# Optimization experiments

Hardware: AMD Instinct MI355X
Metric: run time of the kernel (lower is better)

Reference implementation:

```python
import jax, jax.numpy as jnp
import numpy as np

# Module configuration (matches init_kwargs)
B = 128           # batch
C = 21            # in_channels
L = 2048          # in_features
W = 32            # window_size
S = 8             # strides
O = 16            # out_channels
EPS = 1e-6
M = int((L - W) / S - EPS)      # number of regularly-strided windows (251)
NW = M + 1                       # total windows incl. clamped last one (252)
NK = O * NW                      # 4032
# window start positions: j*S for j<M, last window clamped to L-W
STARTS = np.concatenate([np.arange(M) * S, np.array([L - W])]).astype(np.int32)


def setup_inputs() -> dict:
    key = jax.random.key(0)
    kx, kw = jax.random.split(key)
    x = jax.random.normal(kx, (B, C, L), dtype=jnp.float32)
    # original init: 2*(rand-0.5)/sqrt(W*C), uniform in [-1,1]/sqrt(W*C)
    weight = (2.0 * (jax.random.uniform(kw, (NK, W * C), dtype=jnp.float32) - 0.5)
              / np.sqrt(W * C).astype(np.float32))
    return {"x": x, "weight": weight}


def reference(x, weight):
    # im2col gather implied by the sparse fbank: patches[b,c,j,w] = x[b,c,starts[j]+w]
    idx = jnp.asarray(STARTS)[:, None] + jnp.arange(W)[None, :]   # (NW, W)
    patches = x[:, :, idx]                                        # (B, C, NW, W)
    # weight rows are n = j*O + o, columns laid out k*W + w (channel-major)
    w4 = weight.reshape(NW, O, C, W)                              # (NW, O, C, W)
    # h[b, j*O+o] = sum_{c,w} patches[b,c,j,w] * w4[j,o,c,w]
    h = jnp.einsum('bcjw,jocw->bjo', patches, w4)                 # (B, NW, O)
    return h.reshape(B, NK)
```

## Files before the change

kernel.cpp:

```cpp
#include <hip/hip_runtime.h>
#include <hip/hip_bf16.h>

#define Bb   128
#define Cc   21
#define Ll   2048
#define Ss   8
#define Oo   16
#define NWw  252
#define NKk  4032
#define Kk   672
#define KP   680

typedef __attribute__((ext_vector_type(8))) short  short8;
typedef __attribute__((ext_vector_type(4))) float  f32x4;

static __device__ __forceinline__ unsigned short f2bf(float f) {
    union { __hip_bfloat16 h; unsigned short u; } cv;
    cv.h = __float2bfloat16(f);
    return cv.u;
}

__global__ __launch_bounds__(256)
void cvt_x(const float* __restrict__ x, unsigned short* __restrict__ xb) {
    const int total4 = Bb * Cc * Ll / 4;
    for (int t = blockIdx.x * 256 + threadIdx.x; t < total4;
         t += gridDim.x * 256) {
        float4 v = ((const float4*)x)[t];
        ushort4 p = make_ushort4(f2bf(v.x), f2bf(v.y), f2bf(v.z), f2bf(v.w));
        ((ushort4*)xb)[t] = p;
    }
}

__global__ __launch_bounds__(512)
void fb_mm(const unsigned short* __restrict__ xb, const float* __restrict__ w,
           float* __restrict__ out) {
    __shared__ unsigned short ws[Oo * KP];

    const int bid = blockIdx.x;
    const int j   = (bid & 7) * 32 + (bid >> 3);
    if (j >= NWw) return;
    const int s    = (j < NWw - 1) ? j * Ss : (Ll - 32);
    const int tid  = threadIdx.x;
    const int lane = tid & 63;
    const int wv   = tid >> 6;
    const int col  = lane & 15;
    const int quad = lane >> 4;

    {
        const float4* wj4 = (const float4*)(w + (size_t)j * Oo * Kk);
        for (int t = tid; t < Oo * (Kk / 4); t += 512) {
            float4 v = wj4[t];
            int o = t / (Kk / 4);
            int r = t - o * (Kk / 4);
            ushort4 p = make_ushort4(f2bf(v.x), f2bf(v.y), f2bf(v.z), f2bf(v.w));
            *(ushort4*)&ws[o * KP + r * 4] = p;
        }
    }

    const unsigned short* xrow =
        xb + ((size_t)(wv * 16 + col) * Cc) * Ll + s + quad * 8;
    short8 afr[Cc];
#pragma unroll
    for (int c = 0; c < Cc; ++c)
        afr[c] = *(const short8*)(xrow + (size_t)c * Ll);

    __syncthreads();

    const unsigned short* wrow = &ws[col * KP + quad * 8];
    f32x4 acc = {0.f, 0.f, 0.f, 0.f};
#pragma unroll
    for (int c = 0; c < Cc; ++c)
        acc = __builtin_amdgcn_mfma_f32_16x16x32_bf16(
            afr[c], *(const short8*)(wrow + c * 32), acc, 0, 0, 0);

    const int rbase = wv * 16 + quad * 4;
    float* op = out + (size_t)rbase * NKk + j * 16 + col;
#pragma unroll
    for (int r = 0; r < 4; ++r)
        op[(size_t)r * NKk] = acc[r];
}

extern "C" void kernel_launch(void* const* d_in, const int* in_sizes, int n_in,
                              void* d_out, int out_size, void* d_ws, size_t ws_size,
                              hipStream_t stream) {
    const float* x = (const float*)d_in[0];
    const float* w = (const float*)d_in[1];
    float* out = (float*)d_out;
    unsigned short* xb = (unsigned short*)d_ws;
    cvt_x<<<dim3(1344), dim3(256), 0, stream>>>(x, xb);
    fb_mm<<<dim3(256), dim3(512), 0, stream>>>(xb, w, out);
}
```

Measured before the change: 84.44 us.

## Pre-convert weights to bf16, DMA them into LDS, split batch across blocks

The weight fp32→bf16 conversion moves out of the matmul kernel into a combined conversion pre-pass that writes bf16 weights to workspace. The matmul kernel then fills LDS directly with global_load_lds 16-byte transfers, and the batch is split into two halves so twice as many 256-thread blocks run. The aim is to shorten the serial per-block weight staging and raise parallelism in the main kernel. The cost is an extra write and re-read of the bf16 weight copy, and each weight slice is now loaded by two blocks.

```diff
diff --git a/kernel.cpp b/kernel.cpp
--- a/kernel.cpp
+++ b/kernel.cpp
@@ -21,24 +21,35 @@
 }
 
 __global__ __launch_bounds__(256)
-void cvt_x(const float* __restrict__ x, unsigned short* __restrict__ xb) {
-    const int total4 = Bb * Cc * Ll / 4;
-    for (int t = blockIdx.x * 256 + threadIdx.x; t < total4;
-         t += gridDim.x * 256) {
+void cvt_all(const float* __restrict__ x, const float* __restrict__ w,
+             unsigned short* __restrict__ xb, unsigned short* __restrict__ wb) {
+    const int nx4 = Bb * Cc * Ll / 4;
+    const int nw4 = NKk * Kk / 4;
+    const int t0 = blockIdx.x * 256 + threadIdx.x;
+    const int st = gridDim.x * 256;
+    for (int t = t0; t < nx4; t += st) {
         float4 v = ((const float4*)x)[t];
-        ushort4 p = make_ushort4(f2bf(v.x), f2bf(v.y), f2bf(v.z), f2bf(v.w));
-        ((ushort4*)xb)[t] = p;
+        ((ushort4*)xb)[t] = make_ushort4(f2bf(v.x), f2bf(v.y), f2bf(v.z), f2bf(v.w));
+    }
+    for (int t = t0; t < nw4; t += st) {
+        float4 v = ((const float4*)w)[t];
+        ((ushort4*)wb)[t] = make_ushort4(f2bf(v.x), f2bf(v.y), f2bf(v.z), f2bf(v.w));
     }
 }
 
-__global__ __launch_bounds__(512)
-void fb_mm(const unsigned short* __restrict__ xb, const float* __restrict__ w,
+__global__ __launch_bounds__(256, 2)
+void fb_mm(const unsigned short* __restrict__ xb,
+           const unsigned short* __restrict__ wb,
            float* __restrict__ out) {
-    __shared__ unsigned short ws[Oo * KP];
+    __shared__ unsigned short ws[22 * 512];
 
     const int bid = blockIdx.x;
-    const int j   = (bid & 7) * 32 + (bid >> 3);
+    const int r   = bid & 7;
+    const int t2  = bid >> 3;
+    const int j   = r * 32 + (t2 >> 1);
+    const int bh  = t2 & 1;
     if (j >= NWw) return;
+
     const int s    = (j < NWw - 1) ? j * Ss : (Ll - 32);
     const int tid  = threadIdx.x;
     const int lane = tid & 63;
@@ -47,18 +58,21 @@
     const int quad = lane >> 4;
 
     {
-        const float4* wj4 = (const float4*)(w + (size_t)j * Oo * Kk);
-        for (int t = tid; t < Oo * (Kk / 4); t += 512) {
-            float4 v = wj4[t];
-            int o = t / (Kk / 4);
-            int r = t - o * (Kk / 4);
-            ushort4 p = make_ushort4(f2bf(v.x), f2bf(v.y), f2bf(v.z), f2bf(v.w));
-            *(ushort4*)&ws[o * KP + r * 4] = p;
+        const unsigned short* wj = wb + (size_t)j * (Oo * Kk);
+        for (int iss = wv; iss < 22; iss += 4) {
+            int g  = iss * 64 + lane;
+            int ro = g / 85;  if (ro > 15) ro = 15;
+            int co = g - ro * 85; if (co > 83) co = 83;
+            const unsigned short* src = wj + ro * Kk + co * 8;
+            __builtin_amdgcn_global_load_lds(
+                (const __attribute__((address_space(1))) void*)src,
+                (__attribute__((address_space(3))) void*)&ws[iss * 512],
+                16, 0, 0);
         }
     }
 
     const unsigned short* xrow =
-        xb + ((size_t)(wv * 16 + col) * Cc) * Ll + s + quad * 8;
+        xb + ((size_t)(bh * 64 + wv * 16 + col) * Cc) * Ll + s + quad * 8;
     short8 afr[Cc];
 #pragma unroll
     for (int c = 0; c < Cc; ++c)
@@ -73,11 +87,11 @@
         acc = __builtin_amdgcn_mfma_f32_16x16x32_bf16(
             afr[c], *(const short8*)(wrow + c * 32), acc, 0, 0, 0);
 
-    const int rbase = wv * 16 + quad * 4;
+    const int rbase = bh * 64 + wv * 16 + quad * 4;
     float* op = out + (size_t)rbase * NKk + j * 16 + col;
 #pragma unroll
-    for (int r = 0; r < 4; ++r)
-        op[(size_t)r * NKk] = acc[r];
+    for (int rr = 0; rr < 4; ++rr)
+        op[(size_t)rr * NKk] = acc[rr];
 }
 
 extern "C" void kernel_launch(void* const* d_in, const int* in_sizes, int n_in,
@@ -87,6 +101,7 @@
     const float* w = (const float*)d_in[1];
     float* out = (float*)d_out;
     unsigned short* xb = (unsigned short*)d_ws;
-    cvt_x<<<dim3(1344), dim3(256), 0, stream>>>(x, xb);
-    fb_mm<<<dim3(256), dim3(512), 0, stream>>>(xb, w, out);
+    unsigned short* wb = (unsigned short*)d_ws + (size_t)Bb * Cc * Ll;
+    cvt_all<<<dim3(2048), dim3(256), 0, stream>>>(x, w, xb, wb);
+    fb_mm<<<dim3(512), dim3(256), 0, stream>>>(xb, wb, out);
 }
```

Result: no change. 84.58 us (+0.2%).

## Transpose x into chunk-major bf16 layout so window loads are contiguous

Applied to the files above, without the earlier changes.

The conversion kernel now writes x as bf16 in an 8-element-chunk-major layout (chunk, row, 8), so each window's 32 samples across all batch/channel rows sit contiguously. The matmul kernel's A-fragment loads then read adjacent 16-byte pieces across lanes instead of strided rows, and they are issued before the weight staging so their latency overlaps it. The trade-off is that the transpose kernel's stores are now scattered with a large stride instead of streaming, and its grid is halved.

```diff
diff --git a/kernel.cpp b/kernel.cpp
--- a/kernel.cpp
+++ b/kernel.cpp
@@ -10,6 +10,8 @@
 #define NKk  4032
 #define Kk   672
 #define KP   680
+#define NR   (Bb * Cc)
+#define NCH  (Ll / 8)
 
 typedef __attribute__((ext_vector_type(8))) short  short8;
 typedef __attribute__((ext_vector_type(4))) float  f32x4;
@@ -21,18 +23,25 @@
 }
 
 __global__ __launch_bounds__(256)
-void cvt_x(const float* __restrict__ x, unsigned short* __restrict__ xb) {
-    const int total4 = Bb * Cc * Ll / 4;
-    for (int t = blockIdx.x * 256 + threadIdx.x; t < total4;
+void xpose(const float* __restrict__ x, unsigned short* __restrict__ xt) {
+    const int total = NR * NCH;
+    for (int t = blockIdx.x * 256 + threadIdx.x; t < total;
          t += gridDim.x * 256) {
-        float4 v = ((const float4*)x)[t];
-        ushort4 p = make_ushort4(f2bf(v.x), f2bf(v.y), f2bf(v.z), f2bf(v.w));
-        ((ushort4*)xb)[t] = p;
+        const int row = t >> 8;
+        const int k   = t & 255;
+        const float* src = x + (size_t)row * Ll + k * 8;
+        const float4 v0 = *(const float4*)src;
+        const float4 v1 = *(const float4*)(src + 4);
+        unsigned short* dst = xt + ((size_t)k * NR + row) * 8;
+        *(ushort4*)dst =
+            make_ushort4(f2bf(v0.x), f2bf(v0.y), f2bf(v0.z), f2bf(v0.w));
+        *(ushort4*)(dst + 4) =
+            make_ushort4(f2bf(v1.x), f2bf(v1.y), f2bf(v1.z), f2bf(v1.w));
     }
 }
 
 __global__ __launch_bounds__(512)
-void fb_mm(const unsigned short* __restrict__ xb, const float* __restrict__ w,
+void fb_mm(const unsigned short* __restrict__ xt, const float* __restrict__ w,
            float* __restrict__ out) {
     __shared__ unsigned short ws[Oo * KP];
 
@@ -40,11 +49,20 @@
     const int j   = (bid & 7) * 32 + (bid >> 3);
     if (j >= NWw) return;
     const int s    = (j < NWw - 1) ? j * Ss : (Ll - 32);
+    const int c0   = s >> 3;
     const int tid  = threadIdx.x;
     const int lane = tid & 63;
     const int wv   = tid >> 6;
     const int col  = lane & 15;
     const int quad = lane >> 4;
+
+    const int m = wv * 16 + col;
+    const unsigned short* xrow =
+        xt + ((size_t)(c0 + quad) * NR + (size_t)m * Cc) * 8;
+    short8 afr[Cc];
+#pragma unroll
+    for (int c = 0; c < Cc; ++c)
+        afr[c] = *(const short8*)(xrow + c * 8);
 
     {
         const float4* wj4 = (const float4*)(w + (size_t)j * Oo * Kk);
@@ -52,18 +70,10 @@
             float4 v = wj4[t];
             int o = t / (Kk / 4);
             int r = t - o * (Kk / 4);
-            ushort4 p = make_ushort4(f2bf(v.x), f2bf(v.y), f2bf(v.z), f2bf(v.w));
-            *(ushort4*)&ws[o * KP + r * 4] = p;
+            *(ushort4*)&ws[o * KP + r * 4] =
+                make_ushort4(f2bf(v.x), f2bf(v.y), f2bf(v.z), f2bf(v.w));
         }
     }
-
-    const unsigned short* xrow =
-        xb + ((size_t)(wv * 16 + col) * Cc) * Ll + s + quad * 8;
-    short8 afr[Cc];
-#pragma unroll
-    for (int c = 0; c < Cc; ++c)
-        afr[c] = *(const short8*)(xrow + (size_t)c * Ll);
-
     __syncthreads();
 
     const unsigned short* wrow = &ws[col * KP + quad * 8];
@@ -86,7 +96,7 @@
     const float* x = (const float*)d_in[0];
     const float* w = (const float*)d_in[1];
     float* out = (float*)d_out;
-    unsigned short* xb = (unsigned short*)d_ws;
-    cvt_x<<<dim3(1344), dim3(256), 0, stream>>>(x, xb);
-    fb_mm<<<dim3(256), dim3(512), 0, stream>>>(xb, w, out);
+    unsigned short* xt = (unsigned short*)d_ws;
+    xpose<<<dim3(672), dim3(256), 0, stream>>>(x, xt);
+    fb_mm<<<dim3(256), dim3(512), 0, stream>>>(xt, w, out);
 }
```

Measured after the change: 86.37 us. 1.02x slower.
